# Performance work log

Hardware: AMD Instinct MI355X
Metric: run time of the kernel (lower is better)

The kernel has to match this reference:

```python
import jax, jax.numpy as jnp
import numpy as np

# dims: T timesteps, B batch, IN input, OUT output, H controller hidden,
# N mem slots, C mem cell size, R read heads
T, B, IN, OUT, H, N, C, R = 512, 64, 256, 256, 512, 2048, 64, 4
EPS = 1e-8


def setup_inputs() -> dict:
    key = jax.random.key(0)
    ks = jax.random.split(key, 12)
    s = 0.02
    d_in = IN + C * R  # controller sees x_t concat flattened read vectors
    return {
        "xs": jax.random.normal(ks[0], (T, B, IN), jnp.float32),
        "W_ih": jax.random.normal(ks[1], (d_in, 4 * H), jnp.float32) * s,
        "W_hh": jax.random.normal(ks[2], (H, 4 * H), jnp.float32) * s,
        "b_lstm": jnp.zeros((4 * H,), jnp.float32),
        "W_out": jax.random.normal(ks[3], (H, OUT), jnp.float32) * s,
        "b_out": jnp.zeros((OUT,), jnp.float32),
        "W_key": jax.random.normal(ks[4], (H, C), jnp.float32) * s,
        "b_key": jnp.zeros((C,), jnp.float32),
        "W_beta": jax.random.normal(ks[5], (H, 1), jnp.float32) * s,
        "b_beta": jnp.zeros((1,), jnp.float32),
        "W_gen": jax.random.normal(ks[6], (H, C), jnp.float32) * s,
        "b_gen": jnp.zeros((C,), jnp.float32),
    }


def reference(xs, W_ih, W_hh, b_lstm, W_out, b_out, W_key, b_key,
              W_beta, b_beta, W_gen, b_gen):
    Bx = xs.shape[1]
    mem0 = jnp.zeros((Bx, N, C), xs.dtype)
    h0 = jnp.zeros((Bx, H), xs.dtype)
    c0 = jnp.zeros((Bx, H), xs.dtype)
    rv0 = jnp.zeros((Bx, C, R), xs.dtype)
    sl0 = jnp.zeros((), xs.dtype)

    def step(carry, x_t):
        h, c, mem, rv, sl = carry
        inp = jnp.concatenate([x_t, rv.reshape(Bx, -1)], axis=-1)
        gates = inp @ W_ih + h @ W_hh + b_lstm
        i_g, f_g, g_g, o_g = jnp.split(gates, 4, axis=-1)
        c = jax.nn.sigmoid(f_g) * c + jax.nn.sigmoid(i_g) * jnp.tanh(g_g)
        h = jax.nn.sigmoid(o_g) * jnp.tanh(c)
        pre_out = h @ W_out + b_out                    # (B, OUT)
        key = h @ W_key + b_key                        # (B, C)
        beta = jax.nn.softplus(h @ W_beta + b_beta)    # (B, 1)
        gen = h @ W_gen + b_gen                        # (B, C)
        # cosine similarity between each memory slot and the key
        num = jnp.einsum('bnc,bc->bn', mem, key)
        den = (jnp.maximum(jnp.linalg.norm(mem, axis=-1), EPS)
               * jnp.maximum(jnp.linalg.norm(key, axis=-1, keepdims=True), EPS))
        sim = num / den                                # (B, N)
        w = jax.nn.softmax(beta * sim, axis=-1)        # (B, N)
        # supervised (teacher) loss for this step
        sl = sl + jnp.mean((key - gen) ** 2)
        # additive content write: rank-1 update
        mem = mem + w[:, :, None] * key[:, None, :]
        # read: weights are the write weights repeated over read heads,
        # so all heads read the same vector -> compute once and broadcast
        r = jnp.einsum('bn,bnc->bc', w, mem)           # (B, C)
        rv = jnp.broadcast_to(r[:, :, None], (Bx, C, R))
        return (h, c, mem, rv, sl), pre_out

    (h, c, mem, rv, sup_loss), y_all = jax.lax.scan(
        step, (h0, c0, mem0, rv0, sl0), xs)
    return y_all, sup_loss
```

## Files before the change

### kernel.cpp

```cpp
#include <hip/hip_runtime.h>
#include <hip/hip_fp16.h>

#define EPSF 1e-8f
#define SCOPE_AGT __HIP_MEMORY_SCOPE_AGENT


struct P4 {
  const unsigned* W2h;
  const float* b_lstm;
  const float* W_out;
  const float* b_out;
  const float* W_key;
  const float* b_key;
  const float* W_beta;
  const float* b_beta;
  const float* W_gen;
  const float* b_gen;
  const float* xs;
  float* hbuf;
  float* keyP;
  float* genP;
  float* yP;
  float* betaP;
  float* AccP;
  float* ZP;
  float* S2P;
  unsigned* ctr;
  float* out;
};

__device__ __forceinline__ float sigm(float x) { return 1.f / (1.f + __expf(-x)); }
__device__ __forceinline__ float aload(const float* p) {
  return __hip_atomic_load(p, __ATOMIC_RELAXED, SCOPE_AGT);
}
__device__ __forceinline__ void astore(float* p, float v) {
  __hip_atomic_store(p, v, __ATOMIC_RELAXED, SCOPE_AGT);
}

__global__ void __launch_bounds__(1024, 4) dnc_b4(P4 P) {
  const int tid   = threadIdx.x;
  const int bid   = blockIdx.x;
  const int chunk = (bid >> 1) & 3;
  const int b     = ((bid >> 3) << 1) | (bid & 1);
  const int lane  = tid & 63;
  const int wv    = tid >> 6;
  const int sgrp  = lane >> 4;
  const int c4    = lane & 15;

  __shared__ float s_inp[832];
  __shared__ float s_gates[512];
  __shared__ float s_c[128];
  __shared__ float s_part[4096];
  __shared__ float s_e[512];
  __shared__ float s_key[64], s_kprev[64], s_genv[64];
  __shared__ float s_wred[32];
  __shared__ float s_scal[4];

  unsigned* ctr = P.ctr + b * 32;

  float4 mreg[8];
  float  sden[8];
#pragma unroll
  for (int i = 0; i < 8; ++i) mreg[i] = make_float4(0.f, 0.f, 0.f, 0.f);

  for (int i = 256 + tid; i < 832; i += 1024) s_inp[i] = 0.f;
  if (tid < 128) s_c[tid] = 0.f;
  if (tid < 512) s_e[tid] = 0.f;
  if (tid < 64)  s_kprev[tid] = 0.f;
  float lossacc = 0.f;
  __syncthreads();

  const int q  = tid >> 7;
  const int cg = tid & 127;
  const unsigned* wbase = P.W2h + (size_t)chunk * 212992 + (cg << 2);

  for (int t = 0; t < 512; ++t) {
    if (tid < 128)
      ((float2*)s_inp)[tid] = ((const float2*)P.xs)[((size_t)t * 64 + b) * 128 + tid];
    __syncthreads();

    float4 acc = make_float4(0.f, 0.f, 0.f, 0.f);
    {
      const unsigned* wp = wbase + (size_t)(q * 48) * 512;
      const float* ip = s_inp + q * 96;
#pragma unroll 4
      for (int r = 0; r < 48; ++r) {
        const uint4 w = *(const uint4*)(wp + (size_t)r * 512);
        const float2 v = *(const float2*)(ip + r * 2);
        const __half2* h2 = (const __half2*)&w;
        const float2 f0 = __half22float2(h2[0]), f1 = __half22float2(h2[1]);
        const float2 f2 = __half22float2(h2[2]), f3 = __half22float2(h2[3]);
        acc.x = fmaf(v.x, f0.x, fmaf(v.y, f0.y, acc.x));
        acc.y = fmaf(v.x, f1.x, fmaf(v.y, f1.y, acc.y));
        acc.z = fmaf(v.x, f2.x, fmaf(v.y, f2.y, acc.z));
        acc.w = fmaf(v.x, f3.x, fmaf(v.y, f3.y, acc.w));
      }
    }

    if (t > 0) {
      if (tid == 0) {
        while (__hip_atomic_load(ctr, __ATOMIC_RELAXED, SCOPE_AGT) < 8u * (unsigned)t)
          __builtin_amdgcn_s_sleep(1);
      }
      __syncthreads();
      float a0 = 0.f, a1 = 0.f, a2 = 0.f, a3 = 0.f;
      if (tid < 64) {
        const float* ap = P.AccP + b * 256 + tid;
        a0 = aload(ap); a1 = aload(ap + 64); a2 = aload(ap + 128); a3 = aload(ap + 192);
      } else if (tid == 64) {
        const float* zp = P.ZP + b * 4;
        const float* sp = P.S2P + b * 4;
        const float Z  = aload(zp) + aload(zp + 1) + aload(zp + 2) + aload(zp + 3);
        const float S2 = aload(sp) + aload(sp + 1) + aload(sp + 2) + aload(sp + 3);
        s_scal[0] = 1.f / Z;  s_scal[1] = S2;
      }
      __syncthreads();
      if (tid < 64) {
        const float iZ = s_scal[0];
        s_inp[768 + tid] = iZ * ((a0 + a1 + a2 + a3) + s_scal[1] * iZ * s_kprev[tid]);
      }
      __syncthreads();
    } else {
      if (tid == 64) { s_scal[0] = 0.f; s_scal[1] = 0.f; }
      __syncthreads();
    }

    {
      const unsigned* wp = wbase + (size_t)(384 + q * 4) * 512;
      const float* ip = s_inp + 768 + q * 8;
#pragma unroll
      for (int r = 0; r < 4; ++r) {
        const uint4 w = *(const uint4*)(wp + (size_t)r * 512);
        const float2 v = *(const float2*)(ip + r * 2);
        const __half2* h2 = (const __half2*)&w;
        const float2 f0 = __half22float2(h2[0]), f1 = __half22float2(h2[1]);
        const float2 f2 = __half22float2(h2[2]), f3 = __half22float2(h2[3]);
        acc.x = fmaf(v.x, f0.x, fmaf(v.y, f0.y, acc.x));
        acc.y = fmaf(v.x, f1.x, fmaf(v.y, f1.y, acc.y));
        acc.z = fmaf(v.x, f2.x, fmaf(v.y, f2.y, acc.z));
        acc.w = fmaf(v.x, f3.x, fmaf(v.y, f3.y, acc.w));
      }
    }
    *(float4*)&s_part[(q << 9) + (cg << 2)] = acc;
    __syncthreads();

    if (tid < 512) {
      s_gates[tid] = s_part[tid]        + s_part[512 + tid]  + s_part[1024 + tid] + s_part[1536 + tid]
                   + s_part[2048 + tid] + s_part[2560 + tid] + s_part[3072 + tid] + s_part[3584 + tid];
    }
    __syncthreads();
    if (tid < 128) {
      const int jl = tid, cb = chunk * 128 + jl;
      const float gi = s_gates[jl * 4 + 0] + P.b_lstm[cb];
      const float gf = s_gates[jl * 4 + 1] + P.b_lstm[512 + cb];
      const float gg = s_gates[jl * 4 + 2] + P.b_lstm[1024 + cb];
      const float go = s_gates[jl * 4 + 3] + P.b_lstm[1536 + cb];
      const float cn = sigm(gf) * s_c[jl] + sigm(gi) * tanhf(gg);
      s_c[jl] = cn;
      const float hn = sigm(go) * tanhf(cn);
      s_inp[256 + cb] = hn;
      astore(P.hbuf + b * 512 + cb, hn);
    }
    __syncthreads();

    {
      const float* h = s_inp + 256 + chunk * 128;
      {
        const int isg = tid >> 9, rg = (tid >> 6) & 7, c = tid & 63;
        const float* W = isg ? P.W_gen : P.W_key;
        const float* wp2 = W + (size_t)(chunk * 128 + rg * 16) * 64 + c;
        const float* hh = h + rg * 16;
        float a2 = 0.f;
#pragma unroll
        for (int r2 = 0; r2 < 16; ++r2) a2 = fmaf(hh[r2], wp2[(size_t)r2 * 64], a2);
        s_part[tid] = a2;
      }
      {
        const int rg = tid >> 8, col = tid & 255;
        const float* wp2 = P.W_out + (size_t)(chunk * 128 + rg * 32) * 256 + col;
        const float* hh = h + rg * 32;
        float a2 = 0.f;
#pragma unroll 8
        for (int r2 = 0; r2 < 32; ++r2) a2 = fmaf(hh[r2], wp2[(size_t)r2 * 256], a2);
        s_part[1024 + (rg << 8) + col] = a2;
      }
      {
        float pb = (tid < 128) ? h[tid] * P.W_beta[chunk * 128 + tid] : 0.f;
#pragma unroll
        for (int off = 32; off; off >>= 1) pb += __shfl_down(pb, off);
        if (tid < 128 && lane == 0) s_wred[wv] = pb;
      }
    }
    __syncthreads();
    if (tid < 64) {
      float v = 0.f;
#pragma unroll
      for (int k = 0; k < 8; ++k) v += s_part[k * 64 + tid];
      astore(P.keyP + (b * 4 + chunk) * 64 + tid, v);
    } else if (tid < 128) {
      const int c = tid - 64;
      float v = 0.f;
#pragma unroll
      for (int k = 0; k < 8; ++k) v += s_part[512 + k * 64 + c];
      astore(P.genP + (b * 4 + chunk) * 64 + c, v);
    } else if (tid < 384) {
      const int col = tid - 128;
      astore(P.yP + (b * 4 + chunk) * 256 + col,
             s_part[1024 + col] + s_part[1280 + col] + s_part[1536 + col] + s_part[1792 + col]);
    } else if (tid == 384) {
      astore(P.betaP + b * 4 + chunk, s_wred[0] + s_wred[1]);
    }
    __syncthreads();
    if (tid == 0) __hip_atomic_fetch_add(ctr, 1u, __ATOMIC_RELEASE, SCOPE_AGT);

    {
      const float invZp = s_scal[0];
      const float4 kp4 = ((const float4*)s_kprev)[c4];
      const int nbase = (wv * 4 + sgrp) * 8;
#pragma unroll
      for (int it = 0; it < 8; ++it) {
        float4 m4 = mreg[it];
        const float wpv = s_e[nbase + it] * invZp;
        m4.x = fmaf(wpv, kp4.x, m4.x); m4.y = fmaf(wpv, kp4.y, m4.y);
        m4.z = fmaf(wpv, kp4.z, m4.z); m4.w = fmaf(wpv, kp4.w, m4.w);
        float ssq = m4.x * m4.x + m4.y * m4.y + m4.z * m4.z + m4.w * m4.w;
#pragma unroll
        for (int off = 1; off < 16; off <<= 1) ssq += __shfl_xor(ssq, off);
        sden[it] = fmaxf(sqrtf(ssq), EPSF);
        mreg[it] = m4;
      }
    }

    if (tid == 0) {
      while (__hip_atomic_load(ctr, __ATOMIC_RELAXED, SCOPE_AGT) < 8u * (unsigned)t + 4u)
        __builtin_amdgcn_s_sleep(1);
    }
    __syncthreads();
    if (tid < 64) {
      const float* kp = P.keyP + b * 256 + tid;
      s_key[tid] = aload(kp) + aload(kp + 64) + aload(kp + 128) + aload(kp + 192) + P.b_key[tid];
    } else if (tid < 128) {
      const int c = tid - 64;
      const float* gp = P.genP + b * 256 + c;
      s_genv[c] = aload(gp) + aload(gp + 64) + aload(gp + 128) + aload(gp + 192) + P.b_gen[c];
    } else if (tid < 192) {
      const int col = tid - 128, oc = chunk * 64 + col;
      const float* yp = P.yP + b * 1024 + oc;
      P.out[((size_t)t * 64 + b) * 256 + oc] =
          aload(yp) + aload(yp + 256) + aload(yp + 512) + aload(yp + 768) + P.b_out[oc];
    } else if (tid == 192) {
      const float* bp = P.betaP + b * 4;
      const float s = aload(bp) + aload(bp + 1) + aload(bp + 2) + aload(bp + 3) + P.b_beta[0];
      s_scal[2] = (s > 20.f) ? s : log1pf(__expf(s));
    } else if (tid >= 256 && tid < 640) {
      const int i = tid - 256;
      const int pc = i >> 7;
      const int pcc = pc + (pc >= chunk ? 1 : 0);
      const int jl = i & 127;
      s_inp[256 + pcc * 128 + jl] = aload(P.hbuf + b * 512 + pcc * 128 + jl);
    }
    __syncthreads();
    if (wv == 0) {
      const float kv = s_key[lane];
      float sq = kv * kv;
#pragma unroll
      for (int off = 32; off; off >>= 1) sq += __shfl_down(sq, off);
      if (lane == 0) s_scal[3] = fmaxf(sqrtf(sq), EPSF);
    } else if (wv == 1 && chunk == 0) {
      const float d = s_key[lane] - s_genv[lane];
      float ds = d * d;
#pragma unroll
      for (int off = 32; off; off >>= 1) ds += __shfl_down(ds, off);
      if (lane == 0) lossacc += ds;
    }
    __syncthreads();

    {
      const float beta = s_scal[2], kn = s_scal[3];
      const float4 kk = ((const float4*)s_key)[c4];
      float Zp = 0.f, S2p = 0.f;
      float4 acc4 = make_float4(0.f, 0.f, 0.f, 0.f);
      const int nbase = (wv * 4 + sgrp) * 8;
#pragma unroll
      for (int it = 0; it < 8; ++it) {
        const float4 m4 = mreg[it];
        float num = m4.x * kk.x + m4.y * kk.y + m4.z * kk.z + m4.w * kk.w;
#pragma unroll
        for (int off = 1; off < 16; off <<= 1) num += __shfl_xor(num, off);
        const float e = __expf(beta * (num / (sden[it] * kn)));
        if (c4 == 0) { s_e[nbase + it] = e; Zp += e; S2p += e * e; }
        acc4.x = fmaf(e, m4.x, acc4.x); acc4.y = fmaf(e, m4.y, acc4.y);
        acc4.z = fmaf(e, m4.z, acc4.z); acc4.w = fmaf(e, m4.w, acc4.w);
      }
#pragma unroll
      for (int off = 32; off; off >>= 1) { Zp += __shfl_down(Zp, off); S2p += __shfl_down(S2p, off); }
      if (lane == 0) { s_wred[wv] = Zp; s_wred[16 + wv] = S2p; }
#pragma unroll
      for (int off = 16; off < 64; off <<= 1) {
        acc4.x += __shfl_down(acc4.x, off); acc4.y += __shfl_down(acc4.y, off);
        acc4.z += __shfl_down(acc4.z, off); acc4.w += __shfl_down(acc4.w, off);
      }
      if (lane < 16) ((float4*)s_part)[wv * 16 + lane] = acc4;
    }
    __syncthreads();
    if (tid < 64) {
      float a = 0.f;
#pragma unroll
      for (int w = 0; w < 16; ++w) a += s_part[w * 64 + tid];
      astore(P.AccP + (b * 4 + chunk) * 64 + tid, a);
      s_kprev[tid] = s_key[tid];
    } else if (tid == 64) {
      float Z = 0.f, S2 = 0.f;
#pragma unroll
      for (int k = 0; k < 16; ++k) { Z += s_wred[k]; S2 += s_wred[16 + k]; }
      astore(P.ZP + b * 4 + chunk, Z);
      astore(P.S2P + b * 4 + chunk, S2);
    }
    __syncthreads();
    if (tid == 0) __hip_atomic_fetch_add(ctr, 1u, __ATOMIC_RELEASE, SCOPE_AGT);
  }

  if (chunk == 0 && tid == 64) atomicAdd(P.out + 8388608, lossacc * (1.f / 4096.f));
}

__global__ void build_w2h(const float* __restrict__ W_ih, const float* __restrict__ W_hh,
                          unsigned* __restrict__ W2h) {
  const int id = blockIdx.x * 256 + threadIdx.x;
  if (id >= 851968) return;
  const int chunk = id / 212992;
  const int rem   = id % 212992;
  const int rp    = rem >> 9;
  const int cc    = rem & 511;
  const int jl = cc >> 2, g = cc & 3;
  const int col = g * 512 + chunk * 128 + jl;
  float v[2];
#pragma unroll
  for (int k = 0; k < 2; ++k) {
    const int row = rp * 2 + k;
    if (row < 256)      v[k] = W_ih[(size_t)row * 2048 + col];
    else if (row < 768) v[k] = W_hh[(size_t)(row - 256) * 2048 + col];
    else {
      const float* p0 = W_ih + (size_t)(256 + (row - 768) * 4) * 2048 + col;
      v[k] = p0[0] + p0[2048] + p0[4096] + p0[6144];
    }
  }
  const __half2 h2 = __floats2half2_rn(v[0], v[1]);
  W2h[id] = *(const unsigned*)&h2;
}

extern "C" void kernel_launch(void* const* d_in, const int* in_sizes, int n_in,
                              void* d_out, int out_size, void* d_ws, size_t ws_size,
                              hipStream_t stream) {
  const float* xs     = (const float*)d_in[0];
  const float* W_ih   = (const float*)d_in[1];
  const float* W_hh   = (const float*)d_in[2];
  const float* b_lstm = (const float*)d_in[3];
  const float* W_out  = (const float*)d_in[4];
  const float* b_out  = (const float*)d_in[5];
  const float* W_key  = (const float*)d_in[6];
  const float* b_key  = (const float*)d_in[7];
  const float* W_beta = (const float*)d_in[8];
  const float* b_beta = (const float*)d_in[9];
  const float* W_gen  = (const float*)d_in[10];
  const float* b_gen  = (const float*)d_in[11];
  float* out = (float*)d_out;

  float* ws = (float*)d_ws;
  unsigned* W2h = (unsigned*)ws;
  float* hbuf  = ws     + 851968;
  float* keyP  = hbuf   + 32768;
  float* genP  = keyP   + 16384;
  float* yP    = genP   + 16384;
  float* betaP = yP     + 65536;
  float* AccP  = betaP  + 256;
  float* ZP    = AccP   + 16384;
  float* S2P   = ZP     + 256;
  unsigned* ctr = (unsigned*)(S2P + 256);

  hipMemsetAsync(ctr, 0, 2048 * sizeof(unsigned), stream);
  hipMemsetAsync(out + 8388608, 0, sizeof(float), stream);

  build_w2h<<<dim3(3328), dim3(256), 0, stream>>>(W_ih, W_hh, W2h);

  P4 prm;
  prm.W2h = W2h;      prm.b_lstm = b_lstm;
  prm.W_out = W_out;  prm.b_out = b_out;
  prm.W_key = W_key;  prm.b_key = b_key;
  prm.W_beta = W_beta; prm.b_beta = b_beta;
  prm.W_gen = W_gen;  prm.b_gen = b_gen;
  prm.xs = xs;
  prm.hbuf = hbuf; prm.keyP = keyP; prm.genP = genP; prm.yP = yP; prm.betaP = betaP;
  prm.AccP = AccP; prm.ZP = ZP; prm.S2P = S2P;
  prm.ctr = ctr;  prm.out = out;

  void* kargs[] = { &prm };
  hipLaunchCooperativeKernel(reinterpret_cast<void*>(&dnc_b4),
                             dim3(256), dim3(1024), kargs, 0, stream);
}
```

Before: 13.37 ms.

## Compute head projections redundantly per block, use fp16 dot2 for gate matvec

Each block now computes the key, gen, beta and its own output slice from the full h after the h exchange, rather than computing partial projections and exchanging them through global memory. This drops the keyP/genP/yP/betaP exchange and the work between the two sync points. The gate matvec now keeps its input vector in fp16 and uses the packed fdot2 instruction instead of converting weights to fp32. The next step's x_t is also prefetched during the h exchange. The cost is redundant projection work in every block and lower precision on the LSTM inputs.

```diff
diff --git a/kernel.cpp b/kernel.cpp
--- a/kernel.cpp
+++ b/kernel.cpp
@@ -5,7 +5,9 @@
 #define SCOPE_AGT __HIP_MEMORY_SCOPE_AGENT
 
 
-struct P4 {
+typedef _Float16 h2_t __attribute__((ext_vector_type(2)));
+
+struct P5 {
   const unsigned* W2h;
   const float* b_lstm;
   const float* W_out;
@@ -18,10 +20,6 @@
   const float* b_gen;
   const float* xs;
   float* hbuf;
-  float* keyP;
-  float* genP;
-  float* yP;
-  float* betaP;
   float* AccP;
   float* ZP;
   float* S2P;
@@ -36,8 +34,25 @@
 __device__ __forceinline__ void astore(float* p, float v) {
   __hip_atomic_store(p, v, __ATOMIC_RELAXED, SCOPE_AGT);
 }
-
-__global__ void __launch_bounds__(1024, 4) dnc_b4(P4 P) {
+__device__ __forceinline__ h2_t u2h(unsigned u) {
+  union { unsigned u; h2_t h; } x; x.u = u; return x.h;
+}
+
+#if defined(__has_builtin)
+#if __has_builtin(__builtin_amdgcn_fdot2)
+#define HAVE_FDOT2 1
+#endif
+#endif
+
+__device__ __forceinline__ float dot2acc(h2_t a, h2_t b, float c) {
+#ifdef HAVE_FDOT2
+  return __builtin_amdgcn_fdot2(a, b, c, false);
+#else
+  return fmaf((float)a.x, (float)b.x, fmaf((float)a.y, (float)b.y, c));
+#endif
+}
+
+__global__ void __launch_bounds__(1024, 4) dnc_b5(P5 P) {
   const int tid   = threadIdx.x;
   const int bid   = blockIdx.x;
   const int chunk = (bid >> 1) & 3;
@@ -47,7 +62,8 @@
   const int sgrp  = lane >> 4;
   const int c4    = lane & 15;
 
-  __shared__ float s_inp[832];
+  __shared__ _Float16 s_ih[832];
+  __shared__ float s_h[512];
   __shared__ float s_gates[512];
   __shared__ float s_c[128];
   __shared__ float s_part[4096];
@@ -63,10 +79,15 @@
 #pragma unroll
   for (int i = 0; i < 8; ++i) mreg[i] = make_float4(0.f, 0.f, 0.f, 0.f);
 
-  for (int i = 256 + tid; i < 832; i += 1024) s_inp[i] = 0.f;
-  if (tid < 128) s_c[tid] = 0.f;
-  if (tid < 512) s_e[tid] = 0.f;
-  if (tid < 64)  s_kprev[tid] = 0.f;
+  for (int i = 256 + tid; i < 832; i += 1024) s_ih[i] = (_Float16)0.f;
+  if (tid < 512) { s_h[tid] = 0.f; s_e[tid] = 0.f; }
+  if (tid < 128) {
+    s_c[tid] = 0.f;
+    const float2 xv = ((const float2*)P.xs)[(size_t)b * 128 + tid];
+    h2_t hv; hv.x = (_Float16)xv.x; hv.y = (_Float16)xv.y;
+    *(h2_t*)&s_ih[tid * 2] = hv;
+  }
+  if (tid < 64) s_kprev[tid] = 0.f;
   float lossacc = 0.f;
   __syncthreads();
 
@@ -75,25 +96,18 @@
   const unsigned* wbase = P.W2h + (size_t)chunk * 212992 + (cg << 2);
 
   for (int t = 0; t < 512; ++t) {
-    if (tid < 128)
-      ((float2*)s_inp)[tid] = ((const float2*)P.xs)[((size_t)t * 64 + b) * 128 + tid];
-    __syncthreads();
-
     float4 acc = make_float4(0.f, 0.f, 0.f, 0.f);
     {
       const unsigned* wp = wbase + (size_t)(q * 48) * 512;
-      const float* ip = s_inp + q * 96;
+      const _Float16* ip = s_ih + q * 96;
 #pragma unroll 4
       for (int r = 0; r < 48; ++r) {
         const uint4 w = *(const uint4*)(wp + (size_t)r * 512);
-        const float2 v = *(const float2*)(ip + r * 2);
-        const __half2* h2 = (const __half2*)&w;
-        const float2 f0 = __half22float2(h2[0]), f1 = __half22float2(h2[1]);
-        const float2 f2 = __half22float2(h2[2]), f3 = __half22float2(h2[3]);
-        acc.x = fmaf(v.x, f0.x, fmaf(v.y, f0.y, acc.x));
-        acc.y = fmaf(v.x, f1.x, fmaf(v.y, f1.y, acc.y));
-        acc.z = fmaf(v.x, f2.x, fmaf(v.y, f2.y, acc.z));
-        acc.w = fmaf(v.x, f3.x, fmaf(v.y, f3.y, acc.w));
+        const h2_t v = *(const h2_t*)(ip + r * 2);
+        acc.x = dot2acc(u2h(w.x), v, acc.x);
+        acc.y = dot2acc(u2h(w.y), v, acc.y);
+        acc.z = dot2acc(u2h(w.z), v, acc.z);
+        acc.w = dot2acc(u2h(w.w), v, acc.w);
       }
     }
 
@@ -102,8 +116,10 @@
         while (__hip_atomic_load(ctr, __ATOMIC_RELAXED, SCOPE_AGT) < 8u * (unsigned)t)
           __builtin_amdgcn_s_sleep(1);
       }
-      __syncthreads();
-      float a0 = 0.f, a1 = 0.f, a2 = 0.f, a3 = 0.f;
+    }
+    __syncthreads();
+    float a0 = 0.f, a1 = 0.f, a2 = 0.f, a3 = 0.f;
+    if (t > 0) {
       if (tid < 64) {
         const float* ap = P.AccP + b * 256 + tid;
         a0 = aload(ap); a1 = aload(ap + 64); a2 = aload(ap + 128); a3 = aload(ap + 192);
@@ -114,31 +130,28 @@
         const float S2 = aload(sp) + aload(sp + 1) + aload(sp + 2) + aload(sp + 3);
         s_scal[0] = 1.f / Z;  s_scal[1] = S2;
       }
-      __syncthreads();
-      if (tid < 64) {
-        const float iZ = s_scal[0];
-        s_inp[768 + tid] = iZ * ((a0 + a1 + a2 + a3) + s_scal[1] * iZ * s_kprev[tid]);
-      }
-      __syncthreads();
-    } else {
-      if (tid == 64) { s_scal[0] = 0.f; s_scal[1] = 0.f; }
-      __syncthreads();
-    }
+    } else if (tid == 64) {
+      s_scal[0] = 0.f; s_scal[1] = 0.f;
+    }
+    __syncthreads();
+    if (t > 0 && tid < 64) {
+      const float iZ = s_scal[0];
+      const float r = iZ * ((a0 + a1 + a2 + a3) + s_scal[1] * iZ * s_kprev[tid]);
+      s_ih[768 + tid] = (_Float16)r;
+    }
+    __syncthreads();
 
     {
       const unsigned* wp = wbase + (size_t)(384 + q * 4) * 512;
-      const float* ip = s_inp + 768 + q * 8;
+      const _Float16* ip = s_ih + 768 + q * 8;
 #pragma unroll
       for (int r = 0; r < 4; ++r) {
         const uint4 w = *(const uint4*)(wp + (size_t)r * 512);
-        const float2 v = *(const float2*)(ip + r * 2);
-        const __half2* h2 = (const __half2*)&w;
-        const float2 f0 = __half22float2(h2[0]), f1 = __half22float2(h2[1]);
-        const float2 f2 = __half22float2(h2[2]), f3 = __half22float2(h2[3]);
-        acc.x = fmaf(v.x, f0.x, fmaf(v.y, f0.y, acc.x));
-        acc.y = fmaf(v.x, f1.x, fmaf(v.y, f1.y, acc.y));
-        acc.z = fmaf(v.x, f2.x, fmaf(v.y, f2.y, acc.z));
-        acc.w = fmaf(v.x, f3.x, fmaf(v.y, f3.y, acc.w));
+        const h2_t v = *(const h2_t*)(ip + r * 2);
+        acc.x = dot2acc(u2h(w.x), v, acc.x);
+        acc.y = dot2acc(u2h(w.y), v, acc.y);
+        acc.z = dot2acc(u2h(w.z), v, acc.z);
+        acc.w = dot2acc(u2h(w.w), v, acc.w);
       }
     }
     *(float4*)&s_part[(q << 9) + (cg << 2)] = acc;
@@ -158,57 +171,9 @@
       const float cn = sigm(gf) * s_c[jl] + sigm(gi) * tanhf(gg);
       s_c[jl] = cn;
       const float hn = sigm(go) * tanhf(cn);
-      s_inp[256 + cb] = hn;
+      s_h[cb] = hn;
+      s_ih[256 + cb] = (_Float16)hn;
       astore(P.hbuf + b * 512 + cb, hn);
-    }
-    __syncthreads();
-
-    {
-      const float* h = s_inp + 256 + chunk * 128;
-      {
-        const int isg = tid >> 9, rg = (tid >> 6) & 7, c = tid & 63;
-        const float* W = isg ? P.W_gen : P.W_key;
-        const float* wp2 = W + (size_t)(chunk * 128 + rg * 16) * 64 + c;
-        const float* hh = h + rg * 16;
-        float a2 = 0.f;
-#pragma unroll
-        for (int r2 = 0; r2 < 16; ++r2) a2 = fmaf(hh[r2], wp2[(size_t)r2 * 64], a2);
-        s_part[tid] = a2;
-      }
-      {
-        const int rg = tid >> 8, col = tid & 255;
-        const float* wp2 = P.W_out + (size_t)(chunk * 128 + rg * 32) * 256 + col;
-        const float* hh = h + rg * 32;
-        float a2 = 0.f;
-#pragma unroll 8
-        for (int r2 = 0; r2 < 32; ++r2) a2 = fmaf(hh[r2], wp2[(size_t)r2 * 256], a2);
-        s_part[1024 + (rg << 8) + col] = a2;
-      }
-      {
-        float pb = (tid < 128) ? h[tid] * P.W_beta[chunk * 128 + tid] : 0.f;
-#pragma unroll
-        for (int off = 32; off; off >>= 1) pb += __shfl_down(pb, off);
-        if (tid < 128 && lane == 0) s_wred[wv] = pb;
-      }
-    }
-    __syncthreads();
-    if (tid < 64) {
-      float v = 0.f;
-#pragma unroll
-      for (int k = 0; k < 8; ++k) v += s_part[k * 64 + tid];
-      astore(P.keyP + (b * 4 + chunk) * 64 + tid, v);
-    } else if (tid < 128) {
-      const int c = tid - 64;
-      float v = 0.f;
-#pragma unroll
-      for (int k = 0; k < 8; ++k) v += s_part[512 + k * 64 + c];
-      astore(P.genP + (b * 4 + chunk) * 64 + c, v);
-    } else if (tid < 384) {
-      const int col = tid - 128;
-      astore(P.yP + (b * 4 + chunk) * 256 + col,
-             s_part[1024 + col] + s_part[1280 + col] + s_part[1536 + col] + s_part[1792 + col]);
-    } else if (tid == 384) {
-      astore(P.betaP + b * 4 + chunk, s_wred[0] + s_wred[1]);
     }
     __syncthreads();
     if (tid == 0) __hip_atomic_fetch_add(ctr, 1u, __ATOMIC_RELEASE, SCOPE_AGT);
@@ -236,28 +201,70 @@
         __builtin_amdgcn_s_sleep(1);
     }
     __syncthreads();
+    if (tid < 384) {
+      const int pc = tid >> 7;
+      const int pcc = pc + (pc >= chunk ? 1 : 0);
+      const int jl = tid & 127;
+      const float hv = aload(P.hbuf + b * 512 + pcc * 128 + jl);
+      s_h[pcc * 128 + jl] = hv;
+      s_ih[256 + pcc * 128 + jl] = (_Float16)hv;
+    } else if (tid < 512 && t < 511) {
+      const int rp = tid - 384;
+      const float2 xv = ((const float2*)P.xs)[((size_t)(t + 1) * 64 + b) * 128 + rp];
+      h2_t hv; hv.x = (_Float16)xv.x; hv.y = (_Float16)xv.y;
+      *(h2_t*)&s_ih[rp * 2] = hv;
+    }
+    __syncthreads();
+
+    {
+      {
+        const int rg = tid >> 7, cl = tid & 127;
+        const float* W = (cl < 64) ? (P.W_key + cl) : (P.W_gen + (cl - 64));
+        const float* hh = s_h + rg * 64;
+        float a2 = 0.f;
+#pragma unroll 8
+        for (int r2 = 0; r2 < 64; ++r2) a2 = fmaf(hh[r2], W[(size_t)(rg * 64 + r2) * 64], a2);
+        s_part[rg * 128 + cl] = a2;
+      }
+      {
+        const int rg = tid >> 6, col = tid & 63;
+        const float* wp2 = P.W_out + (size_t)(rg * 32) * 256 + chunk * 64 + col;
+        const float* hh = s_h + rg * 32;
+        float a2 = 0.f;
+#pragma unroll 8
+        for (int r2 = 0; r2 < 32; ++r2) a2 = fmaf(hh[r2], wp2[(size_t)r2 * 256], a2);
+        s_part[1024 + (rg << 6) + col] = a2;
+      }
+      {
+        float pb = (tid < 512) ? s_h[tid] * P.W_beta[tid] : 0.f;
+#pragma unroll
+        for (int off = 32; off; off >>= 1) pb += __shfl_down(pb, off);
+        if (tid < 512 && lane == 0) s_wred[wv] = pb;
+      }
+    }
+    __syncthreads();
     if (tid < 64) {
-      const float* kp = P.keyP + b * 256 + tid;
-      s_key[tid] = aload(kp) + aload(kp + 64) + aload(kp + 128) + aload(kp + 192) + P.b_key[tid];
+      float v = 0.f;
+#pragma unroll
+      for (int k = 0; k < 8; ++k) v += s_part[k * 128 + tid];
+      s_key[tid] = v + P.b_key[tid];
     } else if (tid < 128) {
       const int c = tid - 64;
-      const float* gp = P.genP + b * 256 + c;
-      s_genv[c] = aload(gp) + aload(gp + 64) + aload(gp + 128) + aload(gp + 192) + P.b_gen[c];
+      float v = 0.f;
+#pragma unroll
+      for (int k = 0; k < 8; ++k) v += s_part[k * 128 + 64 + c];
+      s_genv[c] = v + P.b_gen[c];
     } else if (tid < 192) {
       const int col = tid - 128, oc = chunk * 64 + col;
-      const float* yp = P.yP + b * 1024 + oc;
-      P.out[((size_t)t * 64 + b) * 256 + oc] =
-          aload(yp) + aload(yp + 256) + aload(yp + 512) + aload(yp + 768) + P.b_out[oc];
+      float v = 0.f;
+#pragma unroll
+      for (int k = 0; k < 16; ++k) v += s_part[1024 + k * 64 + col];
+      P.out[((size_t)t * 64 + b) * 256 + oc] = v + P.b_out[oc];
     } else if (tid == 192) {
-      const float* bp = P.betaP + b * 4;
-      const float s = aload(bp) + aload(bp + 1) + aload(bp + 2) + aload(bp + 3) + P.b_beta[0];
+      float s = P.b_beta[0];
+#pragma unroll
+      for (int k = 0; k < 8; ++k) s += s_wred[k];
       s_scal[2] = (s > 20.f) ? s : log1pf(__expf(s));
-    } else if (tid >= 256 && tid < 640) {
-      const int i = tid - 256;
-      const int pc = i >> 7;
-      const int pcc = pc + (pc >= chunk ? 1 : 0);
-      const int jl = i & 127;
-      s_inp[256 + pcc * 128 + jl] = aload(P.hbuf + b * 512 + pcc * 128 + jl);
     }
     __syncthreads();
     if (wv == 0) {
@@ -344,8 +351,8 @@
       v[k] = p0[0] + p0[2048] + p0[4096] + p0[6144];
     }
   }
-  const __half2 h2 = __floats2half2_rn(v[0], v[1]);
-  W2h[id] = *(const unsigned*)&h2;
+  const __half2 h2v = __floats2half2_rn(v[0], v[1]);
+  W2h[id] = *(const unsigned*)&h2v;
 }
 
 extern "C" void kernel_launch(void* const* d_in, const int* in_sizes, int n_in,
@@ -368,11 +375,7 @@
   float* ws = (float*)d_ws;
   unsigned* W2h = (unsigned*)ws;
   float* hbuf  = ws     + 851968;
-  float* keyP  = hbuf   + 32768;
-  float* genP  = keyP   + 16384;
-  float* yP    = genP   + 16384;
-  float* betaP = yP     + 65536;
-  float* AccP  = betaP  + 256;
+  float* AccP  = hbuf   + 32768;
   float* ZP    = AccP   + 16384;
   float* S2P   = ZP     + 256;
   unsigned* ctr = (unsigned*)(S2P + 256);
@@ -382,18 +385,17 @@
 
   build_w2h<<<dim3(3328), dim3(256), 0, stream>>>(W_ih, W_hh, W2h);
 
-  P4 prm;
+  P5 prm;
   prm.W2h = W2h;      prm.b_lstm = b_lstm;
   prm.W_out = W_out;  prm.b_out = b_out;
   prm.W_key = W_key;  prm.b_key = b_key;
   prm.W_beta = W_beta; prm.b_beta = b_beta;
   prm.W_gen = W_gen;  prm.b_gen = b_gen;
   prm.xs = xs;
-  prm.hbuf = hbuf; prm.keyP = keyP; prm.genP = genP; prm.yP = yP; prm.betaP = betaP;
-  prm.AccP = AccP; prm.ZP = ZP; prm.S2P = S2P;
+  prm.hbuf = hbuf; prm.AccP = AccP; prm.ZP = ZP; prm.S2P = S2P;
   prm.ctr = ctr;  prm.out = out;
 
   void* kargs[] = { &prm };
-  hipLaunchCooperativeKernel(reinterpret_cast<void*>(&dnc_b4),
+  hipLaunchCooperativeKernel(reinterpret_cast<void*>(&dnc_b5),
                              dim3(256), dim3(1024), kargs, 0, stream);
 }
```

Result: no change. 13.59 ms (+1.7%).
